# Kernel optimization log

Hardware: AMD Instinct MI355X
Metric: run time of the kernel (lower is better)

Reference implementation:

```python
import jax, jax.numpy as jnp
import numpy as np

LN_EPS = 1e-5
NEG = -1e9


def _layernorm(x, g, b):
    m = jnp.mean(x, axis=-1, keepdims=True)
    v = jnp.mean(jnp.square(x - m), axis=-1, keepdims=True)
    return (x - m) * jax.lax.rsqrt(v + LN_EPS) * g + b


def setup_inputs() -> dict:
    key = jax.random.key(0)
    ks = jax.random.split(key, 16)
    B, S, E, H, D = 4, 2048, 1024, 16, 64
    s = 0.02
    return {
        "x": jax.random.normal(ks[0], (B, S, E), jnp.float32),
        "mask": jax.random.randint(ks[1], (B, S), 0, 2, jnp.int32),
        "Wq": jax.random.normal(ks[2], (H, E, D), jnp.float32) * s,
        "bq": jnp.zeros((H, D), jnp.float32),
        "Wk": jax.random.normal(ks[3], (H, E, D), jnp.float32) * s,
        "bk": jnp.zeros((H, D), jnp.float32),
        "Wv": jax.random.normal(ks[4], (H, E, D), jnp.float32) * s,
        "bv": jnp.zeros((H, D), jnp.float32),
        "Wo": jax.random.normal(ks[5], (H * D, E), jnp.float32) * s,
        "bo": jnp.zeros((E,), jnp.float32),
        "g1": jnp.ones((E,), jnp.float32),
        "b1": jnp.zeros((E,), jnp.float32),
        "W1": jax.random.normal(ks[6], (E, D), jnp.float32) * s,
        "c1": jnp.zeros((D,), jnp.float32),
        "W2": jax.random.normal(ks[7], (D, E), jnp.float32) * s,
        "c2": jnp.zeros((E,), jnp.float32),
        "g2": jnp.ones((E,), jnp.float32),
        "b2": jnp.zeros((E,), jnp.float32),
    }


def reference(x, mask, Wq, bq, Wk, bk, Wv, bv, Wo, bo, g1, b1, W1, c1, W2, c2, g2, b2):
    B, S, E = x.shape
    # per-head projections, batched over heads: [B,H,S,D]
    q = jnp.einsum('bse,hed->bhsd', x, Wq) + bq[None, :, None, :]
    k = jnp.einsum('bse,hed->bhsd', x, Wk) + bk[None, :, None, :]
    v = jnp.einsum('bse,hed->bhsd', x, Wv) + bv[None, :, None, :]
    # NOTE: original scales by sqrt(seq_len) (query.size(1)), not sqrt(head_dim)
    scale = jnp.asarray(S, x.dtype) ** 0.5
    scores = jnp.einsum('bhsd,bhtd->bhst', q, k) / scale
    scores = jnp.where(mask[:, None, None, :] == 0, NEG, scores)
    attn = jax.nn.softmax(scores, axis=-1)
    ctx = jnp.einsum('bhst,bhtd->bhsd', attn, v)
    # concat heads: [B,S,H*D]
    ctx = ctx.transpose(0, 2, 1, 3).reshape(B, S, -1)
    h = _layernorm(ctx @ Wo + bo, g1, b1)
    # bottleneck FFN (dropout = identity at eval), exact GELU
    f = jax.nn.gelu(h @ W1 + c1, approximate=False) @ W2 + c2
    # no residual connection in the original module
    return _layernorm(f, g2, b2)
```

## Files before the change

### kernel.cpp

```cpp
#include <hip/hip_runtime.h>
#include <math.h>

#define B_ 4
#define S_ 2048
#define E_ 1024
#define H_ 16
#define D_ 64
#define M_ (B_*S_)
#define QSCALE (0.022097086912079608f * 1.4426950408889634f)

typedef __bf16 bf16_t;
typedef __bf16 bf16x8 __attribute__((ext_vector_type(8)));
typedef float  f32x4  __attribute__((ext_vector_type(4)));

__device__ __forceinline__ void gload_lds16(const void* g, void* l) {
    __builtin_amdgcn_global_load_lds(
        (const __attribute__((address_space(1))) void*)g,
        (__attribute__((address_space(3))) void*)l, 16, 0, 0);
}
__device__ __forceinline__ bf16x8 ldsx8(const void* p) {
    return __builtin_bit_cast(bf16x8, *(const uint4*)p);
}
__device__ __forceinline__ unsigned short bf16bits(float x) {
    return __builtin_bit_cast(unsigned short, (bf16_t)x);
}
template<int N> __device__ __forceinline__ void waitv() {
    if constexpr (N == 8)      asm volatile("s_waitcnt vmcnt(8) lgkmcnt(0)" ::: "memory");
    else if constexpr (N == 4) asm volatile("s_waitcnt vmcnt(4) lgkmcnt(0)" ::: "memory");
    else if constexpr (N == 3) asm volatile("s_waitcnt vmcnt(3) lgkmcnt(0)" ::: "memory");
    else if constexpr (N == 2) asm volatile("s_waitcnt vmcnt(2) lgkmcnt(0)" ::: "memory");
    else                       asm volatile("s_waitcnt vmcnt(0) lgkmcnt(0)" ::: "memory");
}
__device__ __forceinline__ int fk(int row) { return ((row & 3) + 2 * ((row >> 3) & 3)) & 7; }

template<int BM, int BN, int MODE>
__global__ __launch_bounds__(256) void gemm_bf16(
    const bf16_t* __restrict__ A, const bf16_t* __restrict__ Bt,
    bf16_t* __restrict__ ob0, bf16_t* __restrict__ ob1, bf16_t* __restrict__ ob2,
    const float* __restrict__ bias0, const float* __restrict__ bias1,
    const int* __restrict__ sidx, const int* __restrict__ nkv,
    const int* __restrict__ bmap,
    int M, int N, int K)
{
    constexpr int FM = BM / 32, FN = BN / 32;
    constexpr int NL = BM / 32 + BN / 32;
    constexpr int NBUF = (MODE == 2) ? 1 : 2;
    __shared__ bf16_t As[NBUF][BM * 64];
    __shared__ bf16_t Bs[NBUF][BN * 64];

    const int tid = threadIdx.x;
    const int w   = tid >> 6;
    const int wr  = w >> 1, wc = w & 1;
    const int lr  = tid & 15;
    const int lg  = (tid >> 4) & 3;

    int bm, bn;
    if constexpr (MODE == 2) {
        const int flat = blockIdx.y * gridDim.x + blockIdx.x;
        const int nab = nkv[4];
        const int st = flat >> 7, wfl = flat & 127;
        const int ab = st * 8 + (wfl & 7);
        if (ab >= nab) return;
        const int col = wfl >> 3;
        const int ent = bmap[ab];
        bm = ((ent >> 8) << 11) + (ent & 255) * BM;
        bn = col * BN;
    } else {
        const int nwg = gridDim.x * gridDim.y;
        int bidf = blockIdx.y * gridDim.x + blockIdx.x;
        bidf = (bidf & 7) * (nwg >> 3) + (bidf >> 3);
        bm = (bidf / gridDim.x) * BM;
        bn = (bidf % gridDim.x) * BN;
    }

    int arow[FM];
    if constexpr (MODE == 2) {
        const int b2 = bm >> 11, rbase = bm & 2047;
        #pragma unroll
        for (int i = 0; i < FM; ++i) {
            const int row = (i * 256 + tid) >> 3;
            arow[i] = (b2 << 11) + sidx[(b2 << 11) + rbase + row];
        }
    } else {
        #pragma unroll
        for (int i = 0; i < FM; ++i)
            arow[i] = bm + ((i * 256 + tid) >> 3);
    }

    f32x4 acc[FM][FN] = {};

    auto STAGE = [&](int buf, int kk) {
        #pragma unroll
        for (int i = 0; i < BM / 32; ++i) {
            int idx = i * 256 + tid;
            int row = idx >> 3, slot = idx & 7;
            gload_lds16(A + (size_t)arow[i] * K + kk + (slot ^ (row & 7)) * 8,
                        (char*)As[buf] + idx * 16);
        }
        #pragma unroll
        for (int i = 0; i < BN / 32; ++i) {
            int idx = i * 256 + tid;
            int row = idx >> 3, slot = idx & 7;
            gload_lds16(Bt + (size_t)(bn + row) * K + kk + (slot ^ (row & 7)) * 8,
                        (char*)Bs[buf] + idx * 16);
        }
    };

    auto COMPUTE = [&](int buf) {
        #pragma unroll
        for (int h = 0; h < 2; ++h) {
            bf16x8 af[FM], bfr[FN];
            #pragma unroll
            for (int m = 0; m < FM; ++m) {
                int row = wr * (BM / 2) + m * 16 + lr;
                af[m] = ldsx8((char*)As[buf] + row * 128 + (((4 * h + lg) ^ (row & 7)) << 4));
            }
            #pragma unroll
            for (int n = 0; n < FN; ++n) {
                int col = wc * (BN / 2) + n * 16 + lr;
                bfr[n] = ldsx8((char*)Bs[buf] + col * 128 + (((4 * h + lg) ^ (col & 7)) << 4));
            }
            #pragma unroll
            for (int m = 0; m < FM; ++m)
                #pragma unroll
                for (int n = 0; n < FN; ++n)
                    acc[m][n] = __builtin_amdgcn_mfma_f32_16x16x32_bf16(
                        af[m], bfr[n], acc[m][n], 0, 0, 0);
        }
    };

    if constexpr (NBUF == 1) {
        for (int kk = 0; kk < K; kk += 64) {
            __syncthreads();
            STAGE(0, kk);
            __syncthreads();
            COMPUTE(0);
        }
    } else {
        STAGE(0, 0);
        int cur = 0;
        for (int kk = 0; kk < K; kk += 64) {
            if (kk + 64 < K) {
                STAGE(cur ^ 1, kk + 64);
                waitv<NL>();
            } else {
                waitv<0>();
            }
            __builtin_amdgcn_s_barrier();
            COMPUTE(cur);
            __builtin_amdgcn_s_barrier();
            cur ^= 1;
        }
    }

    #pragma unroll
    for (int n = 0; n < FN; ++n) {
        const int gcol = bn + wc * (BN / 2) + n * 16 + lr;
        if constexpr (MODE == 2) {
            const int p = gcol >> 10, nn = gcol & 1023;
            const int b2 = bm >> 11;
            const float bvl = p ? bias1[nn] : bias0[nn];
            #pragma unroll
            for (int m = 0; m < FM; ++m) {
                const int ci0 = (bm & 2047) + wr * (BM / 2) + m * 16 + lg * 4;
                if (p) {
                    ushort4 o;
                    o.x = bf16bits(acc[m][n][0] + bvl);
                    o.y = bf16bits(acc[m][n][1] + bvl);
                    o.z = bf16bits(acc[m][n][2] + bvl);
                    o.w = bf16bits(acc[m][n][3] + bvl);
                    *(ushort4*)(ob2 + ((((size_t)b2 << 10) + nn) << 11) + ci0) = o;
                } else {
                    #pragma unroll
                    for (int r = 0; r < 4; ++r)
                        ob1[((size_t)((b2 << 11) + ci0 + r) << 10) + nn] =
                            (bf16_t)(acc[m][n][r] + bvl);
                }
            }
        } else {
            const float bvl = bias0[gcol];
            #pragma unroll
            for (int m = 0; m < FM; ++m)
                #pragma unroll
                for (int r = 0; r < 4; ++r) {
                    const int grow = bm + wr * (BM / 2) + m * 16 + lg * 4 + r;
                    float v = acc[m][n][r] + bvl;
                    if constexpr (MODE == 1)
                        v = 0.5f * v * (1.0f + erff(v * 0.70710678118654752f));
                    ob0[(size_t)grow * N + gcol] = (bf16_t)v;
                }
        }
    }
}

__global__ __launch_bounds__(256) void compact_mask(
    const int* __restrict__ mask, int* __restrict__ sidx, int* __restrict__ nkv,
    int* __restrict__ bmap)
{
    __shared__ int wsum[4];
    __shared__ int nkp_s[4];
    const int tid = threadIdx.x;
    const int lane = tid & 63, wv = tid >> 6;
    const int base = tid * 8;

    for (int b = 0; b < 4; ++b) {
        int m[8], loc[8];
        int cnt = 0;
        #pragma unroll
        for (int j = 0; j < 8; ++j) {
            m[j] = mask[b * S_ + base + j];
            loc[j] = cnt;
            cnt += (m[j] != 0);
        }
        int incl = cnt;
        #pragma unroll
        for (int off = 1; off < 64; off <<= 1) {
            int t = __shfl_up(incl, off);
            if (lane >= off) incl += t;
        }
        if (lane == 63) wsum[wv] = incl;
        const int excl_lane = incl - cnt;
        __syncthreads();
        int wbase = 0;
        for (int i = 0; i < wv; ++i) wbase += wsum[i];
        const int total = wsum[0] + wsum[1] + wsum[2] + wsum[3];
        if (tid == 0) { nkv[b] = total; nkp_s[b] = (total + 127) & ~127; }
        const int tbase = wbase + excl_lane;
        #pragma unroll
        for (int j = 0; j < 8; ++j)
            if (m[j]) sidx[b * S_ + tbase + loc[j]] = base + j;
        const int nkp = (total + 127) & ~127;
        for (int c = total + tid; c < nkp; c += 256)
            sidx[b * S_ + c] = 0;
        __syncthreads();
    }

    if (tid == 0) {
        int idx = 0;
        for (int b = 0; b < 4; ++b)
            for (int rb = 0; rb < (nkp_s[b] >> 7); ++rb)
                bmap[idx++] = (b << 8) | rb;
        nkv[4] = idx;
    }
}

__global__ __launch_bounds__(512) void attn_mfma(
    const bf16_t* __restrict__ qg, const bf16_t* __restrict__ kg,
    const bf16_t* __restrict__ vg, const int* __restrict__ nkv,
    bf16_t* __restrict__ ctx)
{
    __shared__ bf16_t ks[2][64 * 64];
    __shared__ bf16_t vts[2][64 * 64];

    const int tid = threadIdx.x;
    const int w   = tid >> 6;
    const int lr  = tid & 15;
    const int lg  = (tid >> 4) & 3;

    const int bid = blockIdx.x;
    const int xcd = bid & 7, kidx = bid >> 3;
    const int bh  = xcd * 8 + (kidx >> 3);
    const int xq  = kidx & 7;
    const int b   = bh >> 4, h = bh & 15;
    const int q0w = xq * 256 + w * 32;

    const int nk = nkv[b];
    const int ntiles = (nk + 63) >> 6;
    const bool hastail = (nk & 63) != 0;

    bf16x8 aq[2][2];
    #pragma unroll
    for (int f = 0; f < 2; ++f) {
        const bf16_t* qp = qg + ((size_t)(b * S_ + q0w + f * 16 + lr) << 10) + h * 64 + lg * 8;
        aq[f][0] = ldsx8(qp);
        aq[f][1] = ldsx8(qp + 32);
    }

    bf16x8 onesf;
    {
        bf16_t o1 = (bf16_t)((lr == 0) ? 1.0f : 0.0f);
        #pragma unroll
        for (int j = 0; j < 8; ++j) onesf[j] = o1;
    }

    int koff[2][2][2], voff[2][4];
    #pragma unroll
    for (int c = 0; c < 2; ++c) {
        #pragma unroll
        for (int kf1 = 0; kf1 < 2; ++kf1) {
            const int row = c * 32 + 8 * (lr >> 2) + 4 * kf1 + (lr & 3);
            const int f = fk(row);
            koff[c][kf1][0] = row * 128 + ((lg ^ f) << 4);
            koff[c][kf1][1] = row * 128 + (((4 + lg) ^ f) << 4);
        }
        #pragma unroll
        for (int n = 0; n < 4; ++n) {
            const int rowv = n * 16 + lr;
            voff[c][n] = rowv * 128 + (((4 * c + lg) ^ (rowv & 7)) << 4);
        }
    }

    const int srow = tid >> 3, sslot = tid & 7;
    const bf16_t* kptr = kg + ((size_t)((b << 11) + srow) << 10) + h * 64
                            + (sslot ^ fk(srow)) * 8;
    const bf16_t* vptr = vg + (((size_t)bh * 64 + srow) << 11)
                            + (sslot ^ (srow & 7)) * 8;
    char* kdst = (char*)ks + tid * 16;
    char* vdst = (char*)vts + tid * 16;

    f32x4 accO[2][4] = {};
    f32x4 accL[2] = {};

    auto STAGE = [&](int buf) {
        const int nb = buf << 13;
        gload_lds16(kptr, kdst + nb);
        gload_lds16(vptr, vdst + nb);
        kptr += (size_t)64 << 10;
        vptr += 64;
    };

    auto COMPUTE = [&](int buf, int t0, bool tl) {
        const char* ksb = (const char*)ks + (buf << 13);
        const char* vsb = (const char*)vts + (buf << 13);
        #pragma unroll
        for (int c = 0; c < 2; ++c) {
            unsigned int pw0[4], pw1[4];
            #pragma unroll
            for (int kf1 = 0; kf1 < 2; ++kf1) {
                bf16x8 a0 = ldsx8(ksb + koff[c][kf1][0]);
                bf16x8 a1 = ldsx8(ksb + koff[c][kf1][1]);
                f32x4 z0 = {}, z1 = {};
                if (tl) {
                    const int keyb = t0 + c * 32 + 8 * lg + 4 * kf1;
                    f32x4 bias;
                    #pragma unroll
                    for (int r = 0; r < 4; ++r)
                        bias[r] = (keyb + r < nk) ? 0.0f : -1.0e9f;
                    z0 = bias; z1 = bias;
                }
                __builtin_amdgcn_s_setprio(1);
                z0 = __builtin_amdgcn_mfma_f32_16x16x32_bf16(a0, aq[0][0], z0, 0, 0, 0);
                z0 = __builtin_amdgcn_mfma_f32_16x16x32_bf16(a1, aq[0][1], z0, 0, 0, 0);
                z1 = __builtin_amdgcn_mfma_f32_16x16x32_bf16(a0, aq[1][0], z1, 0, 0, 0);
                z1 = __builtin_amdgcn_mfma_f32_16x16x32_bf16(a1, aq[1][1], z1, 0, 0, 0);
                __builtin_amdgcn_s_setprio(0);
                const float p00 = __builtin_amdgcn_exp2f(z0[0]);
                const float p01 = __builtin_amdgcn_exp2f(z0[1]);
                const float p02 = __builtin_amdgcn_exp2f(z0[2]);
                const float p03 = __builtin_amdgcn_exp2f(z0[3]);
                const float p10 = __builtin_amdgcn_exp2f(z1[0]);
                const float p11 = __builtin_amdgcn_exp2f(z1[1]);
                const float p12 = __builtin_amdgcn_exp2f(z1[2]);
                const float p13 = __builtin_amdgcn_exp2f(z1[3]);
                pw0[2 * kf1]     = bf16bits(p00) | ((unsigned)bf16bits(p01) << 16);
                pw0[2 * kf1 + 1] = bf16bits(p02) | ((unsigned)bf16bits(p03) << 16);
                pw1[2 * kf1]     = bf16bits(p10) | ((unsigned)bf16bits(p11) << 16);
                pw1[2 * kf1 + 1] = bf16bits(p12) | ((unsigned)bf16bits(p13) << 16);
            }
            uint4 pk0 = {pw0[0], pw0[1], pw0[2], pw0[3]};
            uint4 pk1 = {pw1[0], pw1[1], pw1[2], pw1[3]};
            const bf16x8 pa0 = __builtin_bit_cast(bf16x8, pk0);
            const bf16x8 pa1 = __builtin_bit_cast(bf16x8, pk1);

            __builtin_amdgcn_s_setprio(1);
            #pragma unroll
            for (int n = 0; n < 4; ++n) {
                bf16x8 av = ldsx8(vsb + voff[c][n]);
                accO[0][n] = __builtin_amdgcn_mfma_f32_16x16x32_bf16(av, pa0, accO[0][n], 0, 0, 0);
                accO[1][n] = __builtin_amdgcn_mfma_f32_16x16x32_bf16(av, pa1, accO[1][n], 0, 0, 0);
            }
            accL[0] = __builtin_amdgcn_mfma_f32_16x16x32_bf16(onesf, pa0, accL[0], 0, 0, 0);
            accL[1] = __builtin_amdgcn_mfma_f32_16x16x32_bf16(onesf, pa1, accL[1], 0, 0, 0);
            __builtin_amdgcn_s_setprio(0);
        }
    };

    STAGE(0);
    int cur = 0;
    for (int t = 0; t < ntiles; ++t) {
        if (t + 1 < ntiles) {
            STAGE(cur ^ 1);
            waitv<2>();
        } else {
            waitv<0>();
        }
        __builtin_amdgcn_s_barrier();
        COMPUTE(cur, t * 64, hastail && (t == ntiles - 1));
        __builtin_amdgcn_s_barrier();
        cur ^= 1;
    }

    #pragma unroll
    for (int f = 0; f < 2; ++f) {
        const float inv = 1.0f / __shfl(accL[f][0], lr);
        bf16_t* obase = ctx + ((size_t)(b * S_ + q0w + f * 16 + lr) << 10) + h * 64;
        #pragma unroll
        for (int n = 0; n < 4; ++n) {
            ushort4 o;
            o.x = bf16bits(accO[f][n][0] * inv);
            o.y = bf16bits(accO[f][n][1] * inv);
            o.z = bf16bits(accO[f][n][2] * inv);
            o.w = bf16bits(accO[f][n][3] * inv);
            *(ushort4*)(obase + n * 16 + lg * 4) = o;
        }
    }
}

__global__ __launch_bounds__(256) void prep_all(
    const float* __restrict__ x, bf16_t* __restrict__ xb,
    const float* __restrict__ Wq, const float* __restrict__ Wk,
    const float* __restrict__ Wv, bf16_t* __restrict__ WqkvT,
    const float* __restrict__ Wo, bf16_t* __restrict__ WoT,
    const float* __restrict__ W1, bf16_t* __restrict__ W1T,
    const float* __restrict__ W2, bf16_t* __restrict__ W2T,
    const float* __restrict__ bq, float* __restrict__ bqs)
{
    __shared__ float t[32][33];
    const int tid = threadIdx.x;
    int bid = blockIdx.x;

    if (bid < 4096) {
        int i = bid * 256 + tid;
        float4 a = ((const float4*)x)[i * 2];
        float4 b = ((const float4*)x)[i * 2 + 1];
        unsigned int p0 = bf16bits(a.x) | ((unsigned)bf16bits(a.y) << 16);
        unsigned int p1 = bf16bits(a.z) | ((unsigned)bf16bits(a.w) << 16);
        unsigned int p2 = bf16bits(b.x) | ((unsigned)bf16bits(b.y) << 16);
        unsigned int p3 = bf16bits(b.z) | ((unsigned)bf16bits(b.w) << 16);
        uint4 o = {p0, p1, p2, p3};
        ((uint4*)xb)[i] = o;
        return;
    }
    bid -= 4096;

    if (bid == 4224) {
        #pragma unroll
        for (int j = 0; j < 4; ++j)
            bqs[tid * 4 + j] = bq[tid * 4 + j] * QSCALE;
        return;
    }

    const float* in; bf16_t* out;
    int R, C, c0, r0;
    float scale = 1.0f;
    if (bid < 3072) {
        const int p = bid >> 10, r = bid & 1023;
        const int z = r >> 6, rem = r & 63;
        in  = (p == 0 ? Wq : p == 1 ? Wk : Wv) + z * 65536;
        out = WqkvT + p * 1048576 + z * 65536;
        R = 1024; C = 64;
        c0 = (rem & 1) * 32; r0 = (rem >> 1) * 32;
        if (p == 0) scale = QSCALE;
    } else if (bid < 4096) {
        const int r = bid - 3072;
        in = Wo; out = WoT; R = 1024; C = 1024;
        c0 = (r & 31) * 32; r0 = (r >> 5) * 32;
    } else if (bid < 4160) {
        const int r = bid - 4096;
        in = W1; out = W1T; R = 1024; C = 64;
        c0 = (r & 1) * 32; r0 = (r >> 1) * 32;
    } else {
        const int r = bid - 4160;
        in = W2; out = W2T; R = 64; C = 1024;
        c0 = (r & 31) * 32; r0 = (r >> 5) * 32;
    }

    {
        int rr = tid >> 3, c4 = (tid & 7) * 4;
        float4 v = *(const float4*)&in[(size_t)(r0 + rr) * C + c0 + c4];
        t[rr][c4 + 0] = v.x * scale;
        t[rr][c4 + 1] = v.y * scale;
        t[rr][c4 + 2] = v.z * scale;
        t[rr][c4 + 3] = v.w * scale;
    }
    __syncthreads();
    {
        int c = tid >> 3, r4 = (tid & 7) * 4;
        ushort4 o;
        o.x = bf16bits(t[r4 + 0][c]);
        o.y = bf16bits(t[r4 + 1][c]);
        o.z = bf16bits(t[r4 + 2][c]);
        o.w = bf16bits(t[r4 + 3][c]);
        *(ushort4*)(out + (size_t)(c0 + c) * R + r0 + r4) = o;
    }
}

template<typename InT, typename OutT>
__global__ __launch_bounds__(256) void ln_kernel(
    const InT* __restrict__ in, const float* __restrict__ g,
    const float* __restrict__ bta, OutT* __restrict__ out)
{
    const int row = blockIdx.x;
    const int tid = threadIdx.x;

    float x0, x1, x2, x3;
    if constexpr (sizeof(InT) == 4) {
        float4 xv = ((const float4*)(in + (size_t)row * E_))[tid];
        x0 = xv.x; x1 = xv.y; x2 = xv.z; x3 = xv.w;
    } else {
        ushort4 xv = *(const ushort4*)((const bf16_t*)in + (size_t)row * E_ + tid * 4);
        x0 = (float)__builtin_bit_cast(bf16_t, xv.x);
        x1 = (float)__builtin_bit_cast(bf16_t, xv.y);
        x2 = (float)__builtin_bit_cast(bf16_t, xv.z);
        x3 = (float)__builtin_bit_cast(bf16_t, xv.w);
    }
    float s  = x0 + x1 + x2 + x3;
    float sq = x0 * x0 + x1 * x1 + x2 * x2 + x3 * x3;
    #pragma unroll
    for (int off = 32; off > 0; off >>= 1) {
        s  += __shfl_down(s, off);
        sq += __shfl_down(sq, off);
    }
    __shared__ float ss[4], ssq[4];
    if ((tid & 63) == 0) { ss[tid >> 6] = s; ssq[tid >> 6] = sq; }
    __syncthreads();
    s  = ss[0] + ss[1] + ss[2] + ss[3];
    sq = ssq[0] + ssq[1] + ssq[2] + ssq[3];

    const float mean = s * (1.0f / E_);
    const float var  = sq * (1.0f / E_) - mean * mean;
    const float rstd = rsqrtf(var + 1e-5f);

    float4 gv = ((const float4*)g)[tid];
    float4 bv = ((const float4*)bta)[tid];
    float o0 = (x0 - mean) * rstd * gv.x + bv.x;
    float o1 = (x1 - mean) * rstd * gv.y + bv.y;
    float o2 = (x2 - mean) * rstd * gv.z + bv.z;
    float o3 = (x3 - mean) * rstd * gv.w + bv.w;
    if constexpr (sizeof(OutT) == 4) {
        float4 o = {o0, o1, o2, o3};
        ((float4*)((float*)out + (size_t)row * E_))[tid] = o;
    } else {
        ushort4 o;
        o.x = bf16bits(o0); o.y = bf16bits(o1);
        o.z = bf16bits(o2); o.w = bf16bits(o3);
        *(ushort4*)((bf16_t*)out + (size_t)row * E_ + tid * 4) = o;
    }
}

extern "C" void kernel_launch(void* const* d_in, const int* in_sizes, int n_in,
                              void* d_out, int out_size, void* d_ws, size_t ws_size,
                              hipStream_t stream)
{
    const float* x    = (const float*)d_in[0];
    const int*   mask = (const int*)d_in[1];
    const float* Wq   = (const float*)d_in[2];
    const float* bq   = (const float*)d_in[3];
    const float* Wk   = (const float*)d_in[4];
    const float* bk   = (const float*)d_in[5];
    const float* Wv   = (const float*)d_in[6];
    const float* bv   = (const float*)d_in[7];
    const float* Wo   = (const float*)d_in[8];
    const float* bo   = (const float*)d_in[9];
    const float* g1   = (const float*)d_in[10];
    const float* b1   = (const float*)d_in[11];
    const float* W1   = (const float*)d_in[12];
    const float* c1   = (const float*)d_in[13];
    const float* W2   = (const float*)d_in[14];
    const float* c2   = (const float*)d_in[15];
    const float* g2   = (const float*)d_in[16];
    const float* b2   = (const float*)d_in[17];

    char* W = (char*)d_ws;
    bf16_t* xb    = (bf16_t*)(W + 0);
    bf16_t* WqkvT = (bf16_t*)(W + 16777216);
    bf16_t* WoT   = (bf16_t*)(W + 23068672);
    bf16_t* W1T   = (bf16_t*)(W + 25165824);
    bf16_t* W2T   = (bf16_t*)(W + 25296896);
    bf16_t* qbuf  = (bf16_t*)(W + 25427968);
    bf16_t* kbuf  = (bf16_t*)(W + 42205184);
    bf16_t* vtc   = (bf16_t*)(W + 58982400);
    bf16_t* ctx   = (bf16_t*)(W + 75759616);
    bf16_t* t1b   = (bf16_t*)(W + 25427968);
    bf16_t* hb    = (bf16_t*)(W + 42205184);
    bf16_t* f1b   = (bf16_t*)(W + 0);
    bf16_t* f2b   = (bf16_t*)(W + 58982400);
    int*    sidx  = (int*)(W + 92536832);
    int*    nkv   = (int*)(W + 92569600);
    float*  bqs   = (float*)(W + 92569664);
    int*    bmap  = (int*)(W + 92573760);
    float*  out   = (float*)d_out;

    prep_all<<<8321, 256, 0, stream>>>(x, xb, Wq, Wk, Wv, WqkvT,
                                       Wo, WoT, W1, W1T, W2, W2T, bq, bqs);

    compact_mask<<<1, 256, 0, stream>>>(mask, sidx, nkv, bmap);

    gemm_bf16<128, 128, 0><<<dim3(8, 64), 256, 0, stream>>>(
        xb, WqkvT, qbuf, nullptr, nullptr, bqs, nullptr, nullptr, nullptr,
        nullptr, M_, 1024, 1024);

    gemm_bf16<128, 128, 2><<<dim3(16, 64), 256, 0, stream>>>(
        xb, WqkvT + (1 << 20), nullptr, kbuf, vtc, bk, bv, sidx, nkv,
        bmap, M_, 2048, 1024);

    attn_mfma<<<dim3(512), 512, 0, stream>>>(qbuf, kbuf, vtc, nkv, ctx);

    gemm_bf16<128, 128, 0><<<dim3(8, 64), 256, 0, stream>>>(
        ctx, WoT, t1b, nullptr, nullptr, bo, nullptr, nullptr, nullptr,
        nullptr, M_, 1024, 1024);

    ln_kernel<bf16_t, bf16_t><<<8192, 256, 0, stream>>>(t1b, g1, b1, hb);

    gemm_bf16<32, 64, 1><<<dim3(1, 256), 256, 0, stream>>>(
        hb, W1T, f1b, nullptr, nullptr, c1, nullptr, nullptr, nullptr,
        nullptr, M_, 64, 1024);

    gemm_bf16<128, 128, 0><<<dim3(8, 64), 256, 0, stream>>>(
        f1b, W2T, f2b, nullptr, nullptr, c2, nullptr, nullptr, nullptr,
        nullptr, M_, 1024, 64);

    ln_kernel<bf16_t, float><<<8192, 256, 0, stream>>>(f2b, g2, b2, out);
}
```

Before: 181.7 us.

## Fold first LayerNorm into Wo GEMM stats and W1 GEMM epilogue

```diff
diff --git a/kernel.cpp b/kernel.cpp
--- a/kernel.cpp
+++ b/kernel.cpp
@@ -38,6 +38,7 @@
     const bf16_t* __restrict__ A, const bf16_t* __restrict__ Bt,
     bf16_t* __restrict__ ob0, bf16_t* __restrict__ ob1, bf16_t* __restrict__ ob2,
     const float* __restrict__ bias0, const float* __restrict__ bias1,
+    float* __restrict__ st1, float* __restrict__ st2,
     const int* __restrict__ sidx, const int* __restrict__ nkv,
     const int* __restrict__ bmap,
     int M, int N, int K)
@@ -153,10 +154,10 @@
         }
     }
 
-    #pragma unroll
-    for (int n = 0; n < FN; ++n) {
-        const int gcol = bn + wc * (BN / 2) + n * 16 + lr;
-        if constexpr (MODE == 2) {
+    if constexpr (MODE == 2) {
+        #pragma unroll
+        for (int n = 0; n < FN; ++n) {
+            const int gcol = bn + wc * (BN / 2) + n * 16 + lr;
             const int p = gcol >> 10, nn = gcol & 1023;
             const int b2 = bm >> 11;
             const float bvl = p ? bias1[nn] : bias0[nn];
@@ -177,7 +178,38 @@
                             (bf16_t)(acc[m][n][r] + bvl);
                 }
             }
-        } else {
+        }
+    } else if constexpr (MODE == 6) {
+        #pragma unroll
+        for (int n = 0; n < FN; ++n) {
+            const int gcol = bn + wc * (BN / 2) + n * 16 + lr;
+            const float csn = bias0[gcol], bbn = bias1[gcol];
+            #pragma unroll
+            for (int m = 0; m < FM; ++m)
+                #pragma unroll
+                for (int r = 0; r < 4; ++r) {
+                    const int grow = bm + wr * (BM / 2) + m * 16 + lg * 4 + r;
+                    const float s  = st1[grow];
+                    const float sq = st2[grow];
+                    const float mean = s * (1.0f / 1024.0f);
+                    const float var  = sq * (1.0f / 1024.0f) - mean * mean;
+                    const float rstd = rsqrtf(var + 1e-5f);
+                    float u = rstd * (acc[m][n][r] - mean * csn) + bbn;
+                    u = 0.5f * u * (1.0f + erff(u * 0.70710678118654752f));
+                    ob0[(size_t)grow * N + gcol] = (bf16_t)u;
+                }
+        }
+    } else {
+        float rs[FM][4], rq[FM][4];
+        if constexpr (MODE == 4) {
+            #pragma unroll
+            for (int m = 0; m < FM; ++m)
+                #pragma unroll
+                for (int r = 0; r < 4; ++r) { rs[m][r] = 0.0f; rq[m][r] = 0.0f; }
+        }
+        #pragma unroll
+        for (int n = 0; n < FN; ++n) {
+            const int gcol = bn + wc * (BN / 2) + n * 16 + lr;
             const float bvl = bias0[gcol];
             #pragma unroll
             for (int m = 0; m < FM; ++m)
@@ -185,9 +217,28 @@
                 for (int r = 0; r < 4; ++r) {
                     const int grow = bm + wr * (BM / 2) + m * 16 + lg * 4 + r;
                     float v = acc[m][n][r] + bvl;
-                    if constexpr (MODE == 1)
-                        v = 0.5f * v * (1.0f + erff(v * 0.70710678118654752f));
                     ob0[(size_t)grow * N + gcol] = (bf16_t)v;
+                    if constexpr (MODE == 4) {
+                        rs[m][r] += v;
+                        rq[m][r] += v * v;
+                    }
+                }
+        }
+        if constexpr (MODE == 4) {
+            #pragma unroll
+            for (int m = 0; m < FM; ++m)
+                #pragma unroll
+                for (int r = 0; r < 4; ++r) {
+                    float s = rs[m][r], q = rq[m][r];
+                    s += __shfl_xor(s, 1);  q += __shfl_xor(q, 1);
+                    s += __shfl_xor(s, 2);  q += __shfl_xor(q, 2);
+                    s += __shfl_xor(s, 4);  q += __shfl_xor(q, 4);
+                    s += __shfl_xor(s, 8);  q += __shfl_xor(q, 8);
+                    if (lr == 0) {
+                        const int grow = bm + wr * (BM / 2) + m * 16 + lg * 4 + r;
+                        atomicAdd(&st1[grow], s);
+                        atomicAdd(&st2[grow], q);
+                    }
                 }
         }
     }
@@ -411,11 +462,16 @@
     const float* __restrict__ Wq, const float* __restrict__ Wk,
     const float* __restrict__ Wv, bf16_t* __restrict__ WqkvT,
     const float* __restrict__ Wo, bf16_t* __restrict__ WoT,
-    const float* __restrict__ W1, bf16_t* __restrict__ W1T,
+    const float* __restrict__ W1, bf16_t* __restrict__ W1gT,
     const float* __restrict__ W2, bf16_t* __restrict__ W2T,
-    const float* __restrict__ bq, float* __restrict__ bqs)
+    const float* __restrict__ bq, float* __restrict__ bqs,
+    const float* __restrict__ g1, const float* __restrict__ b1,
+    const float* __restrict__ c1,
+    float* __restrict__ csv, float* __restrict__ bbv,
+    float* __restrict__ s1, float* __restrict__ sq1)
 {
     __shared__ float t[32][33];
+    __shared__ float red[2][4][64];
     const int tid = threadIdx.x;
     int bid = blockIdx.x;
 
@@ -439,8 +495,33 @@
             bqs[tid * 4 + j] = bq[tid * 4 + j] * QSCALE;
         return;
     }
+    if (bid == 4225) {
+        const int n = tid & 63, part = tid >> 6;
+        float csp = 0.0f, bbp = 0.0f;
+        for (int k = part * 256; k < part * 256 + 256; ++k) {
+            const float wv = W1[k * 64 + n];
+            csp += g1[k] * wv;
+            bbp += b1[k] * wv;
+        }
+        red[0][part][n] = csp;
+        red[1][part][n] = bbp;
+        __syncthreads();
+        if (tid < 64) {
+            csv[tid] = red[0][0][tid] + red[0][1][tid] + red[0][2][tid] + red[0][3][tid];
+            bbv[tid] = red[1][0][tid] + red[1][1][tid] + red[1][2][tid] + red[1][3][tid]
+                       + c1[tid];
+        }
+        return;
+    }
+    if (bid >= 4226 && bid < 4258) {
+        const int i = (bid - 4226) * 256 + tid;
+        s1[i] = 0.0f;
+        sq1[i] = 0.0f;
+        return;
+    }
 
     const float* in; bf16_t* out;
+    const float* gvec = nullptr;
     int R, C, c0, r0;
     float scale = 1.0f;
     if (bid < 3072) {
@@ -457,8 +538,9 @@
         c0 = (r & 31) * 32; r0 = (r >> 5) * 32;
     } else if (bid < 4160) {
         const int r = bid - 4096;
-        in = W1; out = W1T; R = 1024; C = 64;
+        in = W1; out = W1gT; R = 1024; C = 64;
         c0 = (r & 1) * 32; r0 = (r >> 1) * 32;
+        gvec = g1;
     } else {
         const int r = bid - 4160;
         in = W2; out = W2T; R = 64; C = 1024;
@@ -467,11 +549,12 @@
 
     {
         int rr = tid >> 3, c4 = (tid & 7) * 4;
+        float sc = gvec ? gvec[r0 + rr] : scale;
         float4 v = *(const float4*)&in[(size_t)(r0 + rr) * C + c0 + c4];
-        t[rr][c4 + 0] = v.x * scale;
-        t[rr][c4 + 1] = v.y * scale;
-        t[rr][c4 + 2] = v.z * scale;
-        t[rr][c4 + 3] = v.w * scale;
+        t[rr][c4 + 0] = v.x * sc;
+        t[rr][c4 + 1] = v.y * sc;
+        t[rr][c4 + 2] = v.z * sc;
+        t[rr][c4 + 3] = v.w * sc;
     }
     __syncthreads();
     {
@@ -485,25 +568,18 @@
     }
 }
 
-template<typename InT, typename OutT>
 __global__ __launch_bounds__(256) void ln_kernel(
-    const InT* __restrict__ in, const float* __restrict__ g,
-    const float* __restrict__ bta, OutT* __restrict__ out)
+    const bf16_t* __restrict__ in, const float* __restrict__ g,
+    const float* __restrict__ bta, float* __restrict__ out)
 {
     const int row = blockIdx.x;
     const int tid = threadIdx.x;
 
-    float x0, x1, x2, x3;
-    if constexpr (sizeof(InT) == 4) {
-        float4 xv = ((const float4*)(in + (size_t)row * E_))[tid];
-        x0 = xv.x; x1 = xv.y; x2 = xv.z; x3 = xv.w;
-    } else {
-        ushort4 xv = *(const ushort4*)((const bf16_t*)in + (size_t)row * E_ + tid * 4);
-        x0 = (float)__builtin_bit_cast(bf16_t, xv.x);
-        x1 = (float)__builtin_bit_cast(bf16_t, xv.y);
-        x2 = (float)__builtin_bit_cast(bf16_t, xv.z);
-        x3 = (float)__builtin_bit_cast(bf16_t, xv.w);
-    }
+    ushort4 xv = *(const ushort4*)(in + (size_t)row * E_ + tid * 4);
+    float x0 = (float)__builtin_bit_cast(bf16_t, xv.x);
+    float x1 = (float)__builtin_bit_cast(bf16_t, xv.y);
+    float x2 = (float)__builtin_bit_cast(bf16_t, xv.z);
+    float x3 = (float)__builtin_bit_cast(bf16_t, xv.w);
     float s  = x0 + x1 + x2 + x3;
     float sq = x0 * x0 + x1 * x1 + x2 * x2 + x3 * x3;
     #pragma unroll
@@ -523,19 +599,12 @@
 
     float4 gv = ((const float4*)g)[tid];
     float4 bv = ((const float4*)bta)[tid];
-    float o0 = (x0 - mean) * rstd * gv.x + bv.x;
-    float o1 = (x1 - mean) * rstd * gv.y + bv.y;
-    float o2 = (x2 - mean) * rstd * gv.z + bv.z;
-    float o3 = (x3 - mean) * rstd * gv.w + bv.w;
-    if constexpr (sizeof(OutT) == 4) {
-        float4 o = {o0, o1, o2, o3};
-        ((float4*)((float*)out + (size_t)row * E_))[tid] = o;
-    } else {
-        ushort4 o;
-        o.x = bf16bits(o0); o.y = bf16bits(o1);
-        o.z = bf16bits(o2); o.w = bf16bits(o3);
-        *(ushort4*)((bf16_t*)out + (size_t)row * E_ + tid * 4) = o;
-    }
+    float4 o;
+    o.x = (x0 - mean) * rstd * gv.x + bv.x;
+    o.y = (x1 - mean) * rstd * gv.y + bv.y;
+    o.z = (x2 - mean) * rstd * gv.z + bv.z;
+    o.w = (x3 - mean) * rstd * gv.w + bv.w;
+    ((float4*)(out + (size_t)row * E_))[tid] = o;
 }
 
 extern "C" void kernel_launch(void* const* d_in, const int* in_sizes, int n_in,
@@ -565,50 +634,52 @@
     bf16_t* xb    = (bf16_t*)(W + 0);
     bf16_t* WqkvT = (bf16_t*)(W + 16777216);
     bf16_t* WoT   = (bf16_t*)(W + 23068672);
-    bf16_t* W1T   = (bf16_t*)(W + 25165824);
+    bf16_t* W1gT  = (bf16_t*)(W + 25165824);
     bf16_t* W2T   = (bf16_t*)(W + 25296896);
     bf16_t* qbuf  = (bf16_t*)(W + 25427968);
     bf16_t* kbuf  = (bf16_t*)(W + 42205184);
     bf16_t* vtc   = (bf16_t*)(W + 58982400);
     bf16_t* ctx   = (bf16_t*)(W + 75759616);
     bf16_t* t1b   = (bf16_t*)(W + 25427968);
-    bf16_t* hb    = (bf16_t*)(W + 42205184);
     bf16_t* f1b   = (bf16_t*)(W + 0);
     bf16_t* f2b   = (bf16_t*)(W + 58982400);
     int*    sidx  = (int*)(W + 92536832);
     int*    nkv   = (int*)(W + 92569600);
     float*  bqs   = (float*)(W + 92569664);
     int*    bmap  = (int*)(W + 92573760);
+    float*  csv   = (float*)(W + 92574016);
+    float*  bbv   = (float*)(W + 92574272);
+    float*  s1    = (float*)(W + 92574528);
+    float*  sq1   = (float*)(W + 92607296);
     float*  out   = (float*)d_out;
 
-    prep_all<<<8321, 256, 0, stream>>>(x, xb, Wq, Wk, Wv, WqkvT,
-                                       Wo, WoT, W1, W1T, W2, W2T, bq, bqs);
+    prep_all<<<8354, 256, 0, stream>>>(x, xb, Wq, Wk, Wv, WqkvT,
+                                       Wo, WoT, W1, W1gT, W2, W2T, bq, bqs,
+                                       g1, b1, c1, csv, bbv, s1, sq1);
 
     compact_mask<<<1, 256, 0, stream>>>(mask, sidx, nkv, bmap);
 
     gemm_bf16<128, 128, 0><<<dim3(8, 64), 256, 0, stream>>>(
         xb, WqkvT, qbuf, nullptr, nullptr, bqs, nullptr, nullptr, nullptr,
-        nullptr, M_, 1024, 1024);
+        nullptr, nullptr, nullptr, M_, 1024, 1024);
 
     gemm_bf16<128, 128, 2><<<dim3(16, 64), 256, 0, stream>>>(
-        xb, WqkvT + (1 << 20), nullptr, kbuf, vtc, bk, bv, sidx, nkv,
-        bmap, M_, 2048, 1024);
+        xb, WqkvT + (1 << 20), nullptr, kbuf, vtc, bk, bv, nullptr, nullptr,
+        sidx, nkv, bmap, M_, 2048, 1024);
 
     attn_mfma<<<dim3(512), 512, 0, stream>>>(qbuf, kbuf, vtc, nkv, ctx);
 
-    gemm_bf16<128, 128, 0><<<dim3(8, 64), 256, 0, stream>>>(
-        ctx, WoT, t1b, nullptr, nullptr, bo, nullptr, nullptr, nullptr,
-        nullptr, M_, 1024, 1024);
-
-    ln_kernel<bf16_t, bf16_t><<<8192, 256, 0, stream>>>(t1b, g1, b1, hb);
-
-    gemm_bf16<32, 64, 1><<<dim3(1, 256), 256, 0, stream>>>(
-        hb, W1T, f1b, nullptr, nullptr, c1, nullptr, nullptr, nullptr,
-        nullptr, M_, 64, 1024);
+    gemm_bf16<128, 128, 4><<<dim3(8, 64), 256, 0, stream>>>(
+        ctx, WoT, t1b, nullptr, nullptr, bo, nullptr, s1, sq1,
+        nullptr, nullptr, nullptr, M_, 1024, 1024);
+
+    gemm_bf16<32, 64, 6><<<dim3(1, 256), 256, 0, stream>>>(
+        t1b, W1gT, f1b, nullptr, nullptr, csv, bbv, s1, sq1,
+        nullptr, nullptr, nullptr, M_, 64, 1024);
 
     gemm_bf16<128, 128, 0><<<dim3(8, 64), 256, 0, stream>>>(
         f1b, W2T, f2b, nullptr, nullptr, c2, nullptr, nullptr, nullptr,
-        nullptr, M_, 1024, 64);
-
-    ln_kernel<bf16_t, float><<<8192, 256, 0, stream>>>(f2b, g2, b2, out);
-}
+        nullptr, nullptr, nullptr, M_, 1024, 64);
+
+    ln_kernel<<<8192, 256, 0, stream>>>(f2b, g2, b2, out);
+}
```

Result: slower. 186.7 us (+2.8%).
